# Optimization experiments

Measured on AMD Instinct MI355X. Metric: run time of the kernel, lower is better.

The kernel has to match this reference:

```python
import jax, jax.numpy as jnp
import numpy as np

DIMS = [11, 20, 20, 30, 30, 40, 40, 40, 20, 10, 1]  # layer widths

def setup_inputs() -> dict:
    key = jax.random.key(0)
    ks = jax.random.split(key, 1 + 2 * (len(DIMS) - 1))
    inp = {"x": jax.random.normal(ks[0], (2000000, 11), dtype=jnp.float32)}
    for i in range(len(DIMS) - 1):
        d_in, d_out = DIMS[i], DIMS[i + 1]
        bound = 1.0 / np.sqrt(d_in)
        inp[f"W{i}"] = jax.random.uniform(ks[1 + 2 * i], (d_out, d_in), dtype=jnp.float32, minval=-bound, maxval=bound)
        inp[f"b{i}"] = jax.random.uniform(ks[2 + 2 * i], (d_out,), dtype=jnp.float32, minval=-bound, maxval=bound)
    return inp

def _swish(x):
    return x * jax.nn.sigmoid(x)

def reference(x, W0, b0, W1, b1, W2, b2, W3, b3, W4, b4, W5, b5, W6, b6, W7, b7, W8, b8, W9, b9):
    Ws = [W0, W1, W2, W3, W4, W5, W6, W7, W8, W9]
    bs = [b0, b1, b2, b3, b4, b5, b6, b7, b8, b9]
    h = x
    for i in range(9):  # 9 Linear+Swish blocks
        h = _swish(h @ Ws[i].T + bs[i])
    h = jax.nn.relu(h @ Ws[9].T + bs[9])  # final Linear(10,1) + ReLU
    return h.reshape(-1)
```

## Files before the change

kernel.cpp:

```cpp
#include <hip/hip_runtime.h>
#include <math.h>


typedef _Float16 half8 __attribute__((ext_vector_type(8)));
typedef _Float16 half4 __attribute__((ext_vector_type(4)));
typedef _Float16 half2 __attribute__((ext_vector_type(2)));
typedef float f32x4 __attribute__((ext_vector_type(4)));

__device__ __forceinline__ float swish_f(float a) {
    float e = __expf(-a);
    return a * __builtin_amdgcn_rcpf(1.0f + e);
}

__device__ __forceinline__ half8 make_frag(const float* __restrict__ W,
                                           const float* __restrict__ b,
                                           int IN, int OUT, int ot, int kt,
                                           int lr, int kg) {
    const int r = ot * 16 + lr;
    half8 h;
#pragma unroll
    for (int e = 0; e < 8; ++e) {
        const int k = kt * 32 + kg * 8 + e;
        float v = 0.0f;
        if (r < OUT) {
            if (k < IN)
                v = W[r * IN + k];
            else if (k == IN)
                v = b[r];
        }
        h[e] = (_Float16)v;
    }
    return h;
}

template <int NOT, int OUT>
__device__ __forceinline__ void epilogue(const f32x4 (&acc)[NOT],
                                         _Float16* act, int lr, int kg) {
    const int kgl = kg & 1;
    const int kgh = kg >> 1;
#pragma unroll
    for (int ot = 0; ot < NOT; ++ot) {
        float v[4];
#pragma unroll
        for (int r = 0; r < 4; ++r) {
            v[r] = swish_f(acc[ot][r]);
            if (ot == OUT / 16 && ot * 16 + kg * 4 + r == OUT) v[r] = 1.0f;
        }
        auto lo = __builtin_amdgcn_cvt_pkrtz(v[0], v[1]);
        auto hi = __builtin_amdgcn_cvt_pkrtz(v[2], v[3]);
        union {
            half4 h4;
            half2 h2[2];
        } u;
        u.h2[0] = __builtin_bit_cast(half2, lo);
        u.h2[1] = __builtin_bit_cast(half2, hi);
        _Float16* p = act + (ot >> 1) * 512 +
                      (((2 * ot + kgh) & 3) * 16 + lr) * 8 + kgl * 4;
        *(half4*)p = u.h4;
    }
}

template <int NOT, int NKT, int OUT>
__device__ __forceinline__ void layer(const _Float16* __restrict__ wb,
                                      _Float16* act, int lane, int lr, int kg,
                                      f32x4 z4) {
    f32x4 acc[NOT];
#pragma unroll
    for (int kt = 0; kt < NKT; ++kt) {
        const half8 bf = *(const half8*)(act + kt * 512 + lane * 8);
#pragma unroll
        for (int ot = 0; ot < NOT; ++ot) {
            const half8 wf =
                *(const half8*)(wb + (ot * NKT + kt) * 512 + lane * 8);
            acc[ot] = __builtin_amdgcn_mfma_f32_16x16x32_f16(
                wf, bf, kt == 0 ? z4 : acc[ot], 0, 0, 0);
        }
    }
    epilogue<NOT, OUT>(acc, act, lr, kg);
}

__global__ __launch_bounds__(256, 4) void longnet_mlp_r7(
    const float* __restrict__ x,
    const float* __restrict__ W0, const float* __restrict__ b0,
    const float* __restrict__ W1, const float* __restrict__ b1,
    const float* __restrict__ W2, const float* __restrict__ b2,
    const float* __restrict__ W3, const float* __restrict__ b3,
    const float* __restrict__ W4, const float* __restrict__ b4,
    const float* __restrict__ W5, const float* __restrict__ b5,
    const float* __restrict__ W6, const float* __restrict__ b6,
    const float* __restrict__ W7, const float* __restrict__ b7,
    const float* __restrict__ W8, const float* __restrict__ b8,
    const float* __restrict__ W9, const float* __restrict__ b9,
    float* __restrict__ out, int n) {
    __shared__ __align__(16) _Float16 s_w[29 * 512];
    __shared__ __align__(16) _Float16 s_act[4 * 1024];

    const int tid = threadIdx.x;
    const int lane = tid & 63;
    const int wave = tid >> 6;
    const int lr = lane & 15;
    const int kg = lane >> 4;

    {
        const float* Wt[10] = {W0, W1, W2, W3, W4, W5, W6, W7, W8, W9};
        const float* bt[10] = {b0, b1, b2, b3, b4, b5, b6, b7, b8, b9};
        const int INs[10] = {11, 20, 20, 30, 30, 40, 40, 40, 20, 10};
        const int OUTs[10] = {20, 20, 30, 30, 40, 40, 40, 20, 10, 1};
        const int NOTs[10] = {2, 2, 2, 2, 3, 3, 3, 2, 1, 1};
        const int NKTs[10] = {1, 1, 1, 1, 1, 2, 2, 2, 1, 1};
        int f = 0;
        for (int L = 0; L < 10; ++L)
            for (int ot = 0; ot < NOTs[L]; ++ot)
                for (int kt = 0; kt < NKTs[L]; ++kt, ++f)
                    if ((f & 3) == wave) {
                        half8 h = make_frag(Wt[L], bt[L], INs[L], OUTs[L], ot,
                                            kt, lr, kg);
                        *(half8*)(s_w + f * 512 + lane * 8) = h;
                    }
    }

    _Float16* act = s_act + wave * 1024;
    {
        int* a32 = (int*)act;
#pragma unroll
        for (int i = 0; i < 8; ++i) a32[i * 64 + lane] = 0;
    }
    __syncthreads();

    const f32x4 z4 = (f32x4){0.f, 0.f, 0.f, 0.f};
    const int ntile = n >> 4;
    const int step = (int)gridDim.x * 4;

    for (int t = blockIdx.x * 4 + wave; t < ntile; t += step) {
        const int row0 = t * 16;

        half8 xb = {};
        if (kg < 2) {
            const float* xr = x + (size_t)(row0 + lr) * 11 + kg * 8;
#pragma unroll
            for (int e = 0; e < 8; ++e) {
                const int k = kg * 8 + e;
                float v = (k < 11) ? xr[e] : ((k == 11) ? 1.0f : 0.0f);
                xb[e] = (_Float16)v;
            }
        }

        {
            f32x4 acc[2];
#pragma unroll
            for (int ot = 0; ot < 2; ++ot) {
                const half8 wf = *(const half8*)(s_w + ot * 512 + lane * 8);
                acc[ot] = __builtin_amdgcn_mfma_f32_16x16x32_f16(wf, xb, z4,
                                                                 0, 0, 0);
            }
            epilogue<2, 20>(acc, act, lr, kg);
        }
        layer<2, 1, 20>(s_w + 2 * 512, act, lane, lr, kg, z4);
        layer<2, 1, 30>(s_w + 4 * 512, act, lane, lr, kg, z4);
        layer<2, 1, 30>(s_w + 6 * 512, act, lane, lr, kg, z4);
        layer<3, 1, 40>(s_w + 8 * 512, act, lane, lr, kg, z4);
        layer<3, 2, 40>(s_w + 11 * 512, act, lane, lr, kg, z4);
        layer<3, 2, 40>(s_w + 17 * 512, act, lane, lr, kg, z4);
        layer<2, 2, 20>(s_w + 23 * 512, act, lane, lr, kg, z4);
        layer<1, 1, 10>(s_w + 27 * 512, act, lane, lr, kg, z4);

        {
            const half8 wf = *(const half8*)(s_w + 28 * 512 + lane * 8);
            const half8 bf = *(const half8*)(act + lane * 8);
            f32x4 accF =
                __builtin_amdgcn_mfma_f32_16x16x32_f16(wf, bf, z4, 0, 0, 0);
            if (kg == 0) out[row0 + lr] = fmaxf(accF[0], 0.0f);
        }
    }
}

extern "C" void kernel_launch(void* const* d_in, const int* in_sizes, int n_in,
                              void* d_out, int out_size, void* d_ws, size_t ws_size,
                              hipStream_t stream) {
    const float* x = (const float*)d_in[0];
    const float* W0 = (const float*)d_in[1];
    const float* b0 = (const float*)d_in[2];
    const float* W1 = (const float*)d_in[3];
    const float* b1 = (const float*)d_in[4];
    const float* W2 = (const float*)d_in[5];
    const float* b2 = (const float*)d_in[6];
    const float* W3 = (const float*)d_in[7];
    const float* b3 = (const float*)d_in[8];
    const float* W4 = (const float*)d_in[9];
    const float* b4 = (const float*)d_in[10];
    const float* W5 = (const float*)d_in[11];
    const float* b5 = (const float*)d_in[12];
    const float* W6 = (const float*)d_in[13];
    const float* b6 = (const float*)d_in[14];
    const float* W7 = (const float*)d_in[15];
    const float* b7 = (const float*)d_in[16];
    const float* W8 = (const float*)d_in[17];
    const float* b8 = (const float*)d_in[18];
    const float* W9 = (const float*)d_in[19];
    const float* b9 = (const float*)d_in[20];
    float* out = (float*)d_out;

    const int n = in_sizes[0] / 11;
    const int grid = 1024;

    longnet_mlp_r7<<<grid, 256, 0, stream>>>(
        x, W0, b0, W1, b1, W2, b2, W3, b3, W4, b4, W5, b5, W6, b6, W7, b7, W8,
        b8, W9, b9, out, n);
}
```

Baseline: 196.8 us.

## Process two 16-row tiles per wave to interleave independent MFMA chains

Each wave now handles a pair of 16-row tiles, issuing two independent MFMA chains that share each weight fragment load, with a separate activation buffer per tile. This is meant to hide MFMA and LDS latency in the serial layer chain through instruction-level parallelism, and to halve the weight-fragment LDS reads per row. The grid is also reduced to 768 blocks. It doubles activation LDS and accumulator registers, which may lower occupancy, and rows beyond a multiple of 32 are now dropped (n=2M is divisible, so correct here).

```diff
diff --git a/kernel.cpp b/kernel.cpp
--- a/kernel.cpp
+++ b/kernel.cpp
@@ -61,25 +61,44 @@
 }
 
 template <int NOT, int NKT, int OUT>
-__device__ __forceinline__ void layer(const _Float16* __restrict__ wb,
-                                      _Float16* act, int lane, int lr, int kg,
-                                      f32x4 z4) {
-    f32x4 acc[NOT];
+__device__ __forceinline__ void layer2(const _Float16* __restrict__ wb,
+                                       _Float16* act0, _Float16* act1,
+                                       int lane, int lr, int kg, f32x4 z4) {
+    f32x4 acc0[NOT], acc1[NOT];
 #pragma unroll
     for (int kt = 0; kt < NKT; ++kt) {
-        const half8 bf = *(const half8*)(act + kt * 512 + lane * 8);
+        const half8 bf0 = *(const half8*)(act0 + kt * 512 + lane * 8);
+        const half8 bf1 = *(const half8*)(act1 + kt * 512 + lane * 8);
 #pragma unroll
         for (int ot = 0; ot < NOT; ++ot) {
             const half8 wf =
                 *(const half8*)(wb + (ot * NKT + kt) * 512 + lane * 8);
-            acc[ot] = __builtin_amdgcn_mfma_f32_16x16x32_f16(
-                wf, bf, kt == 0 ? z4 : acc[ot], 0, 0, 0);
-        }
-    }
-    epilogue<NOT, OUT>(acc, act, lr, kg);
-}
-
-__global__ __launch_bounds__(256, 4) void longnet_mlp_r7(
+            acc0[ot] = __builtin_amdgcn_mfma_f32_16x16x32_f16(
+                wf, bf0, kt == 0 ? z4 : acc0[ot], 0, 0, 0);
+            acc1[ot] = __builtin_amdgcn_mfma_f32_16x16x32_f16(
+                wf, bf1, kt == 0 ? z4 : acc1[ot], 0, 0, 0);
+        }
+    }
+    epilogue<NOT, OUT>(acc0, act0, lr, kg);
+    epilogue<NOT, OUT>(acc1, act1, lr, kg);
+}
+
+__device__ __forceinline__ half8 load_xb(const float* __restrict__ x,
+                                         int row0, int lr, int kg) {
+    half8 xb = {};
+    if (kg < 2) {
+        const float* xr = x + (size_t)(row0 + lr) * 11 + kg * 8;
+#pragma unroll
+        for (int e = 0; e < 8; ++e) {
+            const int k = kg * 8 + e;
+            float v = (k < 11) ? xr[e] : ((k == 11) ? 1.0f : 0.0f);
+            xb[e] = (_Float16)v;
+        }
+    }
+    return xb;
+}
+
+__global__ __launch_bounds__(256, 4) void longnet_mlp_r8(
     const float* __restrict__ x,
     const float* __restrict__ W0, const float* __restrict__ b0,
     const float* __restrict__ W1, const float* __restrict__ b1,
@@ -93,7 +112,7 @@
     const float* __restrict__ W9, const float* __restrict__ b9,
     float* __restrict__ out, int n) {
     __shared__ __align__(16) _Float16 s_w[29 * 512];
-    __shared__ __align__(16) _Float16 s_act[4 * 1024];
+    __shared__ __align__(16) _Float16 s_act[8 * 1024];
 
     const int tid = threadIdx.x;
     const int lane = tid & 63;
@@ -119,57 +138,59 @@
                     }
     }
 
-    _Float16* act = s_act + wave * 1024;
+    _Float16* act0 = s_act + wave * 2048;
+    _Float16* act1 = act0 + 1024;
     {
-        int* a32 = (int*)act;
-#pragma unroll
-        for (int i = 0; i < 8; ++i) a32[i * 64 + lane] = 0;
+        int* a32 = (int*)act0;
+#pragma unroll
+        for (int i = 0; i < 16; ++i) a32[i * 64 + lane] = 0;
     }
     __syncthreads();
 
     const f32x4 z4 = (f32x4){0.f, 0.f, 0.f, 0.f};
-    const int ntile = n >> 4;
+    const int npair = n >> 5;
     const int step = (int)gridDim.x * 4;
 
-    for (int t = blockIdx.x * 4 + wave; t < ntile; t += step) {
-        const int row0 = t * 16;
-
-        half8 xb = {};
-        if (kg < 2) {
-            const float* xr = x + (size_t)(row0 + lr) * 11 + kg * 8;
-#pragma unroll
-            for (int e = 0; e < 8; ++e) {
-                const int k = kg * 8 + e;
-                float v = (k < 11) ? xr[e] : ((k == 11) ? 1.0f : 0.0f);
-                xb[e] = (_Float16)v;
-            }
-        }
+    for (int t = blockIdx.x * 4 + wave; t < npair; t += step) {
+        const int row0 = t * 32;
+
+        const half8 xb0 = load_xb(x, row0, lr, kg);
+        const half8 xb1 = load_xb(x, row0 + 16, lr, kg);
 
         {
-            f32x4 acc[2];
+            f32x4 acc0[2], acc1[2];
 #pragma unroll
             for (int ot = 0; ot < 2; ++ot) {
                 const half8 wf = *(const half8*)(s_w + ot * 512 + lane * 8);
-                acc[ot] = __builtin_amdgcn_mfma_f32_16x16x32_f16(wf, xb, z4,
-                                                                 0, 0, 0);
+                acc0[ot] = __builtin_amdgcn_mfma_f32_16x16x32_f16(wf, xb0, z4,
+                                                                  0, 0, 0);
+                acc1[ot] = __builtin_amdgcn_mfma_f32_16x16x32_f16(wf, xb1, z4,
+                                                                  0, 0, 0);
             }
-            epilogue<2, 20>(acc, act, lr, kg);
-        }
-        layer<2, 1, 20>(s_w + 2 * 512, act, lane, lr, kg, z4);
-        layer<2, 1, 30>(s_w + 4 * 512, act, lane, lr, kg, z4);
-        layer<2, 1, 30>(s_w + 6 * 512, act, lane, lr, kg, z4);
-        layer<3, 1, 40>(s_w + 8 * 512, act, lane, lr, kg, z4);
-        layer<3, 2, 40>(s_w + 11 * 512, act, lane, lr, kg, z4);
-        layer<3, 2, 40>(s_w + 17 * 512, act, lane, lr, kg, z4);
-        layer<2, 2, 20>(s_w + 23 * 512, act, lane, lr, kg, z4);
-        layer<1, 1, 10>(s_w + 27 * 512, act, lane, lr, kg, z4);
+            epilogue<2, 20>(acc0, act0, lr, kg);
+            epilogue<2, 20>(acc1, act1, lr, kg);
+        }
+        layer2<2, 1, 20>(s_w + 2 * 512, act0, act1, lane, lr, kg, z4);
+        layer2<2, 1, 30>(s_w + 4 * 512, act0, act1, lane, lr, kg, z4);
+        layer2<2, 1, 30>(s_w + 6 * 512, act0, act1, lane, lr, kg, z4);
+        layer2<3, 1, 40>(s_w + 8 * 512, act0, act1, lane, lr, kg, z4);
+        layer2<3, 2, 40>(s_w + 11 * 512, act0, act1, lane, lr, kg, z4);
+        layer2<3, 2, 40>(s_w + 17 * 512, act0, act1, lane, lr, kg, z4);
+        layer2<2, 2, 20>(s_w + 23 * 512, act0, act1, lane, lr, kg, z4);
+        layer2<1, 1, 10>(s_w + 27 * 512, act0, act1, lane, lr, kg, z4);
 
         {
             const half8 wf = *(const half8*)(s_w + 28 * 512 + lane * 8);
-            const half8 bf = *(const half8*)(act + lane * 8);
-            f32x4 accF =
-                __builtin_amdgcn_mfma_f32_16x16x32_f16(wf, bf, z4, 0, 0, 0);
-            if (kg == 0) out[row0 + lr] = fmaxf(accF[0], 0.0f);
+            const half8 bf0 = *(const half8*)(act0 + lane * 8);
+            const half8 bf1 = *(const half8*)(act1 + lane * 8);
+            f32x4 aF0 =
+                __builtin_amdgcn_mfma_f32_16x16x32_f16(wf, bf0, z4, 0, 0, 0);
+            f32x4 aF1 =
+                __builtin_amdgcn_mfma_f32_16x16x32_f16(wf, bf1, z4, 0, 0, 0);
+            if (kg == 0) {
+                out[row0 + lr] = fmaxf(aF0[0], 0.0f);
+                out[row0 + 16 + lr] = fmaxf(aF1[0], 0.0f);
+            }
         }
     }
 }
@@ -201,9 +222,9 @@
     float* out = (float*)d_out;
 
     const int n = in_sizes[0] / 11;
-    const int grid = 1024;
-
-    longnet_mlp_r7<<<grid, 256, 0, stream>>>(
+    const int grid = 768;
+
+    longnet_mlp_r8<<<grid, 256, 0, stream>>>(
         x, W0, b0, W1, b1, W2, b2, W3, b3, W4, b4, W5, b5, W6, b6, W7, b7, W8,
         b8, W9, b9, out, n);
 }
```

New measurement: 208.2 us. 5.8% more time.

## Process two row tiles per wave and use K=16 MFMA for narrow layers

Applied to the files above, without the earlier changes.

Each wave now handles two 16-row tiles per iteration, interleaving their MFMAs so the same weight fragment feeds both and independent work can hide latency. Layers whose K dimension is small, and the 8-column remainder beyond 32, now use 16x16x16 MFMAs instead of padding to a full second 32-wide K tile. The activation buffer in LDS is XOR-swizzled to reduce bank conflicts. The cost is more registers and LDS per wave, which may lower occupancy, plus more complex indexing.

```diff
diff --git a/kernel.cpp b/kernel.cpp
--- a/kernel.cpp
+++ b/kernel.cpp
@@ -7,20 +7,36 @@
 typedef _Float16 half2 __attribute__((ext_vector_type(2)));
 typedef float f32x4 __attribute__((ext_vector_type(4)));
 
+__device__ __forceinline__ int swz(int a) {
+    return a ^ (((a >> 7) & 1) << 4) ^ (((a >> 8) & 1) << 5);
+}
+
 __device__ __forceinline__ float swish_f(float a) {
     float e = __expf(-a);
     return a * __builtin_amdgcn_rcpf(1.0f + e);
 }
 
-__device__ __forceinline__ half8 make_frag(const float* __restrict__ W,
-                                           const float* __restrict__ b,
-                                           int IN, int OUT, int ot, int kt,
-                                           int lr, int kg) {
+__device__ __forceinline__ half4 pack4(const float (&v)[4]) {
+    auto lo = __builtin_amdgcn_cvt_pkrtz(v[0], v[1]);
+    auto hi = __builtin_amdgcn_cvt_pkrtz(v[2], v[3]);
+    union {
+        half4 h4;
+        half2 h2[2];
+    } u;
+    u.h2[0] = __builtin_bit_cast(half2, lo);
+    u.h2[1] = __builtin_bit_cast(half2, hi);
+    return u.h4;
+}
+
+__device__ __forceinline__ half8 make_frag32(const float* __restrict__ W,
+                                             const float* __restrict__ b,
+                                             int IN, int OUT, int ot, int lr,
+                                             int kg) {
     const int r = ot * 16 + lr;
     half8 h;
 #pragma unroll
     for (int e = 0; e < 8; ++e) {
-        const int k = kt * 32 + kg * 8 + e;
+        const int k = kg * 8 + e;
         float v = 0.0f;
         if (r < OUT) {
             if (k < IN)
@@ -33,53 +49,120 @@
     return h;
 }
 
-template <int NOT, int OUT>
-__device__ __forceinline__ void epilogue(const f32x4 (&acc)[NOT],
-                                         _Float16* act, int lr, int kg) {
-    const int kgl = kg & 1;
-    const int kgh = kg >> 1;
+__device__ __forceinline__ half4 make_frag16(const float* __restrict__ W,
+                                             const float* __restrict__ b,
+                                             int IN, int OUT, int ot, int kb,
+                                             int lr, int kg) {
+    const int r = ot * 16 + lr;
+    half4 h;
+#pragma unroll
+    for (int e = 0; e < 4; ++e) {
+        const int k = kb + kg * 4 + e;
+        float v = 0.0f;
+        if (r < OUT) {
+            if (k < IN)
+                v = W[r * IN + k];
+            else if (k == IN)
+                v = b[r];
+        }
+        h[e] = (_Float16)v;
+    }
+    return h;
+}
+
+struct TP {
+    const half8* r0;
+    const half4* r1;
+    _Float16* w0;
+    _Float16* w1;
+    _Float16* wk;
+};
+
+template <int NK0, int MARK, int NOT>
+__device__ __forceinline__ void epi_kt0(const f32x4 (&A)[NOT], const TP& t,
+                                        int kg) {
+#pragma unroll
+    for (int ot = 0; ot < NK0; ++ot) {
+        float v[4];
+#pragma unroll
+        for (int r = 0; r < 4; ++r) {
+            v[r] = swish_f(A[ot][r]);
+            if (ot == MARK / 16 && ot * 16 + kg * 4 + r == MARK) v[r] = 1.0f;
+        }
+        _Float16* wp = (ot == 0) ? t.w0 : t.w1;
+        *(half4*)wp = pack4(v);
+    }
+}
+
+template <int MREL>
+__device__ __forceinline__ void epi_kt1(const f32x4& a, const TP& t, int kg) {
+    float v[4];
+#pragma unroll
+    for (int r = 0; r < 4; ++r) {
+        v[r] = swish_f(a[r]);
+        if constexpr (MREL >= 0) {
+            if (kg * 4 + r == MREL) v[r] = 1.0f;
+        }
+    }
+    *(half4*)t.wk = pack4(v);
+}
+
+template <int NOT, bool K1>
+__device__ __forceinline__ void compute2(const _Float16* __restrict__ w32,
+                                         const _Float16* __restrict__ w16,
+                                         const TP& t0, const TP& t1,
+                                         f32x4 (&A)[NOT], f32x4 (&B)[NOT],
+                                         int lane) {
+    const f32x4 z4 = {0.f, 0.f, 0.f, 0.f};
+    const half8 b0 = *t0.r0;
+    const half8 b1 = *t1.r0;
 #pragma unroll
     for (int ot = 0; ot < NOT; ++ot) {
-        float v[4];
-#pragma unroll
-        for (int r = 0; r < 4; ++r) {
-            v[r] = swish_f(acc[ot][r]);
-            if (ot == OUT / 16 && ot * 16 + kg * 4 + r == OUT) v[r] = 1.0f;
-        }
-        auto lo = __builtin_amdgcn_cvt_pkrtz(v[0], v[1]);
-        auto hi = __builtin_amdgcn_cvt_pkrtz(v[2], v[3]);
-        union {
-            half4 h4;
-            half2 h2[2];
-        } u;
-        u.h2[0] = __builtin_bit_cast(half2, lo);
-        u.h2[1] = __builtin_bit_cast(half2, hi);
-        _Float16* p = act + (ot >> 1) * 512 +
-                      (((2 * ot + kgh) & 3) * 16 + lr) * 8 + kgl * 4;
-        *(half4*)p = u.h4;
-    }
-}
-
-template <int NOT, int NKT, int OUT>
-__device__ __forceinline__ void layer(const _Float16* __restrict__ wb,
-                                      _Float16* act, int lane, int lr, int kg,
-                                      f32x4 z4) {
-    f32x4 acc[NOT];
-#pragma unroll
-    for (int kt = 0; kt < NKT; ++kt) {
-        const half8 bf = *(const half8*)(act + kt * 512 + lane * 8);
+        const half8 wf = *(const half8*)(w32 + ot * 512 + lane * 8);
+        A[ot] = __builtin_amdgcn_mfma_f32_16x16x32_f16(wf, b0, z4, 0, 0, 0);
+        B[ot] = __builtin_amdgcn_mfma_f32_16x16x32_f16(wf, b1, z4, 0, 0, 0);
+    }
+    if constexpr (K1) {
+        const half4 c0 = *t0.r1;
+        const half4 c1 = *t1.r1;
 #pragma unroll
         for (int ot = 0; ot < NOT; ++ot) {
-            const half8 wf =
-                *(const half8*)(wb + (ot * NKT + kt) * 512 + lane * 8);
-            acc[ot] = __builtin_amdgcn_mfma_f32_16x16x32_f16(
-                wf, bf, kt == 0 ? z4 : acc[ot], 0, 0, 0);
-        }
-    }
-    epilogue<NOT, OUT>(acc, act, lr, kg);
-}
-
-__global__ __launch_bounds__(256, 4) void longnet_mlp_r7(
+            const half4 wg = *(const half4*)(w16 + ot * 256 + lane * 4);
+            A[ot] = __builtin_amdgcn_mfma_f32_16x16x16f16(wg, c0, A[ot], 0, 0, 0);
+            B[ot] = __builtin_amdgcn_mfma_f32_16x16x16f16(wg, c1, B[ot], 0, 0, 0);
+        }
+    }
+}
+
+template <int NOT, bool K1, int NK0, int MARK, int MREL>
+__device__ __forceinline__ void layerX(const _Float16* __restrict__ w32,
+                                       const _Float16* __restrict__ w16,
+                                       const TP& t0, const TP& t1, int lane,
+                                       int kg) {
+    f32x4 A[NOT], B[NOT];
+    compute2<NOT, K1>(w32, w16, t0, t1, A, B, lane);
+    epi_kt0<NK0, MARK>(A, t0, kg);
+    epi_kt0<NK0, MARK>(B, t1, kg);
+    if constexpr (NOT > NK0) {
+        epi_kt1<MREL>(A[NK0], t0, kg);
+        epi_kt1<MREL>(B[NK0], t1, kg);
+    }
+}
+
+__device__ __forceinline__ half4 load_x4(const float* __restrict__ x,
+                                         int row0, int lr, int kg) {
+    half4 b = {};
+    const float* xr = x + (size_t)(row0 + lr) * 11;
+#pragma unroll
+    for (int e = 0; e < 4; ++e) {
+        const int k = kg * 4 + e;
+        float v = (k < 11) ? xr[k] : ((k == 11) ? 1.0f : 0.0f);
+        b[e] = (_Float16)v;
+    }
+    return b;
+}
+
+__global__ __launch_bounds__(256, 4) void longnet_mlp_r9(
     const float* __restrict__ x,
     const float* __restrict__ W0, const float* __restrict__ b0,
     const float* __restrict__ W1, const float* __restrict__ b1,
@@ -92,84 +175,104 @@
     const float* __restrict__ W8, const float* __restrict__ b8,
     const float* __restrict__ W9, const float* __restrict__ b9,
     float* __restrict__ out, int n) {
-    __shared__ __align__(16) _Float16 s_w[29 * 512];
-    __shared__ __align__(16) _Float16 s_act[4 * 1024];
+    __shared__ __align__(16) _Float16 s_w[12032];
+    __shared__ __align__(16) _Float16 s_act[6144];
 
     const int tid = threadIdx.x;
     const int lane = tid & 63;
     const int wave = tid >> 6;
     const int lr = lane & 15;
     const int kg = lane >> 4;
+    const int kgl = kg & 1;
+    const int kgh = kg >> 1;
+
+    _Float16* const s_w16 = s_w + 9216;
 
     {
         const float* Wt[10] = {W0, W1, W2, W3, W4, W5, W6, W7, W8, W9};
         const float* bt[10] = {b0, b1, b2, b3, b4, b5, b6, b7, b8, b9};
         const int INs[10] = {11, 20, 20, 30, 30, 40, 40, 40, 20, 10};
         const int OUTs[10] = {20, 20, 30, 30, 40, 40, 40, 20, 10, 1};
-        const int NOTs[10] = {2, 2, 2, 2, 3, 3, 3, 2, 1, 1};
-        const int NKTs[10] = {1, 1, 1, 1, 1, 2, 2, 2, 1, 1};
-        int f = 0;
-        for (int L = 0; L < 10; ++L)
-            for (int ot = 0; ot < NOTs[L]; ++ot)
-                for (int kt = 0; kt < NKTs[L]; ++kt, ++f)
-                    if ((f & 3) == wave) {
-                        half8 h = make_frag(Wt[L], bt[L], INs[L], OUTs[L], ot,
-                                            kt, lr, kg);
-                        *(half8*)(s_w + f * 512 + lane * 8) = h;
-                    }
-    }
-
-    _Float16* act = s_act + wave * 1024;
+        const int L32[18] = {1, 1, 2, 2, 3, 3, 4, 4, 4, 5, 5, 5, 6, 6, 6, 7, 7, 8};
+        const int O32[18] = {0, 1, 0, 1, 0, 1, 0, 1, 2, 0, 1, 2, 0, 1, 2, 0, 1, 0};
+#pragma unroll
+        for (int i = 0; i < 18; ++i)
+            if ((i & 3) == wave) {
+                const int L = L32[i];
+                half8 h = make_frag32(Wt[L], bt[L], INs[L], OUTs[L], O32[i],
+                                      lr, kg);
+                *(half8*)(s_w + i * 512 + lane * 8) = h;
+            }
+        const int L16[11] = {0, 0, 5, 5, 5, 6, 6, 6, 7, 7, 9};
+        const int O16[11] = {0, 1, 0, 1, 2, 0, 1, 2, 0, 1, 0};
+        const int KB16[11] = {0, 0, 32, 32, 32, 32, 32, 32, 32, 32, 0};
+#pragma unroll
+        for (int i = 0; i < 11; ++i)
+            if (((18 + i) & 3) == wave) {
+                const int L = L16[i];
+                half4 h = make_frag16(Wt[L], bt[L], INs[L], OUTs[L], O16[i],
+                                      KB16[i], lr, kg);
+                *(half4*)(s_w16 + i * 256 + lane * 4) = h;
+            }
+    }
+
+    char* const c0 = (char*)s_act + wave * 3072;
+    char* const c1 = c0 + 1536;
+    const int rd0 = swz(lane * 16);
+    const int rk1 = 1024 + lane * 8;
+    const int wo0 = swz((kgh & 3) * 256 + lr * 16 + kgl * 8);
+    const int wo1 = swz(((2 + kgh) & 3) * 256 + lr * 16 + kgl * 8);
+    const TP t0 = {(const half8*)(c0 + rd0), (const half4*)(c0 + rk1),
+                   (_Float16*)(c0 + wo0), (_Float16*)(c0 + wo1),
+                   (_Float16*)(c0 + rk1)};
+    const TP t1 = {(const half8*)(c1 + rd0), (const half4*)(c1 + rk1),
+                   (_Float16*)(c1 + wo0), (_Float16*)(c1 + wo1),
+                   (_Float16*)(c1 + rk1)};
+
     {
-        int* a32 = (int*)act;
-#pragma unroll
-        for (int i = 0; i < 8; ++i) a32[i * 64 + lane] = 0;
+        int* a32 = (int*)c0;
+#pragma unroll
+        for (int i = 0; i < 12; ++i) a32[i * 64 + lane] = 0;
     }
     __syncthreads();
 
-    const f32x4 z4 = (f32x4){0.f, 0.f, 0.f, 0.f};
-    const int ntile = n >> 4;
+    const f32x4 z4 = {0.f, 0.f, 0.f, 0.f};
+    const int npair = n >> 5;
     const int step = (int)gridDim.x * 4;
 
-    for (int t = blockIdx.x * 4 + wave; t < ntile; t += step) {
-        const int row0 = t * 16;
-
-        half8 xb = {};
-        if (kg < 2) {
-            const float* xr = x + (size_t)(row0 + lr) * 11 + kg * 8;
-#pragma unroll
-            for (int e = 0; e < 8; ++e) {
-                const int k = kg * 8 + e;
-                float v = (k < 11) ? xr[e] : ((k == 11) ? 1.0f : 0.0f);
-                xb[e] = (_Float16)v;
+    for (int t = blockIdx.x * 4 + wave; t < npair; t += step) {
+        const int row0 = t * 32;
+
+        {
+            const half4 xb0 = load_x4(x, row0, lr, kg);
+            const half4 xb1 = load_x4(x, row0 + 16, lr, kg);
+            f32x4 A[2], B[2];
+#pragma unroll
+            for (int ot = 0; ot < 2; ++ot) {
+                const half4 wg = *(const half4*)(s_w16 + ot * 256 + lane * 4);
+                A[ot] = __builtin_amdgcn_mfma_f32_16x16x16f16(wg, xb0, z4, 0, 0, 0);
+                B[ot] = __builtin_amdgcn_mfma_f32_16x16x16f16(wg, xb1, z4, 0, 0, 0);
             }
-        }
+            epi_kt0<2, 20>(A, t0, kg);
+            epi_kt0<2, 20>(B, t1, kg);
+        }
+        layerX<2, false, 2, 20, -1>(s_w + 0 * 512, s_w, t0, t1, lane, kg);
+        layerX<2, false, 2, 30, -1>(s_w + 2 * 512, s_w, t0, t1, lane, kg);
+        layerX<2, false, 2, 30, -1>(s_w + 4 * 512, s_w, t0, t1, lane, kg);
+        layerX<3, false, 2, 1000, 8>(s_w + 6 * 512, s_w, t0, t1, lane, kg);
+        layerX<3, true, 2, 1000, 8>(s_w + 9 * 512, s_w16 + 2 * 256, t0, t1, lane, kg);
+        layerX<3, true, 2, 1000, 8>(s_w + 12 * 512, s_w16 + 5 * 256, t0, t1, lane, kg);
+        layerX<2, true, 2, 20, -1>(s_w + 15 * 512, s_w16 + 8 * 256, t0, t1, lane, kg);
+        layerX<1, false, 0, 1000, 10>(s_w + 17 * 512, s_w, t0, t1, lane, kg);
 
         {
-            f32x4 acc[2];
-#pragma unroll
-            for (int ot = 0; ot < 2; ++ot) {
-                const half8 wf = *(const half8*)(s_w + ot * 512 + lane * 8);
-                acc[ot] = __builtin_amdgcn_mfma_f32_16x16x32_f16(wf, xb, z4,
-                                                                 0, 0, 0);
+            const half4 wg = *(const half4*)(s_w16 + 10 * 256 + lane * 4);
+            f32x4 F0 = __builtin_amdgcn_mfma_f32_16x16x16f16(wg, *t0.r1, z4, 0, 0, 0);
+            f32x4 F1 = __builtin_amdgcn_mfma_f32_16x16x16f16(wg, *t1.r1, z4, 0, 0, 0);
+            if (kg == 0) {
+                out[row0 + lr] = fmaxf(F0[0], 0.0f);
+                out[row0 + 16 + lr] = fmaxf(F1[0], 0.0f);
             }
-            epilogue<2, 20>(acc, act, lr, kg);
-        }
-        layer<2, 1, 20>(s_w + 2 * 512, act, lane, lr, kg, z4);
-        layer<2, 1, 30>(s_w + 4 * 512, act, lane, lr, kg, z4);
-        layer<2, 1, 30>(s_w + 6 * 512, act, lane, lr, kg, z4);
-        layer<3, 1, 40>(s_w + 8 * 512, act, lane, lr, kg, z4);
-        layer<3, 2, 40>(s_w + 11 * 512, act, lane, lr, kg, z4);
-        layer<3, 2, 40>(s_w + 17 * 512, act, lane, lr, kg, z4);
-        layer<2, 2, 20>(s_w + 23 * 512, act, lane, lr, kg, z4);
-        layer<1, 1, 10>(s_w + 27 * 512, act, lane, lr, kg, z4);
-
-        {
-            const half8 wf = *(const half8*)(s_w + 28 * 512 + lane * 8);
-            const half8 bf = *(const half8*)(act + lane * 8);
-            f32x4 accF =
-                __builtin_amdgcn_mfma_f32_16x16x32_f16(wf, bf, z4, 0, 0, 0);
-            if (kg == 0) out[row0 + lr] = fmaxf(accF[0], 0.0f);
         }
     }
 }
@@ -203,7 +306,7 @@
     const int n = in_sizes[0] / 11;
     const int grid = 1024;
 
-    longnet_mlp_r7<<<grid, 256, 0, stream>>>(
+    longnet_mlp_r9<<<grid, 256, 0, stream>>>(
         x, W0, b0, W1, b1, W2, b2, W3, b3, W4, b4, W5, b5, W6, b6, W7, b7, W8,
         b8, W9, b9, out, n);
 }
```

Measured after the change: 179.6 us. -8.7%, faster.

## Keep activations in registers via 16x16x16 MFMA and process four tiles per wave

Applied to the files above, without the earlier changes.

Switches from the 16x16x32 MFMA, which needed an LDS round trip to re-layout activations between layers, to the 16x16x16 MFMA. With this instruction the output accumulator layout directly matches the next layer's B-operand layout, so activations stay in registers and the per-wave LDS activation buffer is gone. Each wave now handles four 16-row tiles at once, so each LDS weight fragment load is reused four times and independent MFMAs can interleave. The costs are more K-steps per layer (more, smaller MFMAs), higher register pressure from four tiles of accumulators, and a loop that drops any rows not divisible by 64.

```diff
diff --git a/kernel.cpp b/kernel.cpp
--- a/kernel.cpp
+++ b/kernel.cpp
@@ -2,25 +2,38 @@
 #include <math.h>
 
 
-typedef _Float16 half8 __attribute__((ext_vector_type(8)));
 typedef _Float16 half4 __attribute__((ext_vector_type(4)));
 typedef _Float16 half2 __attribute__((ext_vector_type(2)));
 typedef float f32x4 __attribute__((ext_vector_type(4)));
 
+#define T 4
+
 __device__ __forceinline__ float swish_f(float a) {
     float e = __expf(-a);
     return a * __builtin_amdgcn_rcpf(1.0f + e);
 }
 
-__device__ __forceinline__ half8 make_frag(const float* __restrict__ W,
-                                           const float* __restrict__ b,
-                                           int IN, int OUT, int ot, int kt,
-                                           int lr, int kg) {
+__device__ __forceinline__ half4 pack4(const float (&v)[4]) {
+    auto lo = __builtin_amdgcn_cvt_pkrtz(v[0], v[1]);
+    auto hi = __builtin_amdgcn_cvt_pkrtz(v[2], v[3]);
+    union {
+        half4 h4;
+        half2 h2[2];
+    } u;
+    u.h2[0] = __builtin_bit_cast(half2, lo);
+    u.h2[1] = __builtin_bit_cast(half2, hi);
+    return u.h4;
+}
+
+__device__ __forceinline__ half4 make_frag16(const float* __restrict__ W,
+                                             const float* __restrict__ b,
+                                             int IN, int OUT, int ot, int kb,
+                                             int lr, int kg) {
     const int r = ot * 16 + lr;
-    half8 h;
-#pragma unroll
-    for (int e = 0; e < 8; ++e) {
-        const int k = kt * 32 + kg * 8 + e;
+    half4 h;
+#pragma unroll
+    for (int e = 0; e < 4; ++e) {
+        const int k = kb + kg * 4 + e;
         float v = 0.0f;
         if (r < OUT) {
             if (k < IN)
@@ -33,53 +46,53 @@
     return h;
 }
 
-template <int NOT, int OUT>
-__device__ __forceinline__ void epilogue(const f32x4 (&acc)[NOT],
-                                         _Float16* act, int lr, int kg) {
-    const int kgl = kg & 1;
-    const int kgh = kg >> 1;
-#pragma unroll
-    for (int ot = 0; ot < NOT; ++ot) {
-        float v[4];
-#pragma unroll
-        for (int r = 0; r < 4; ++r) {
-            v[r] = swish_f(acc[ot][r]);
-            if (ot == OUT / 16 && ot * 16 + kg * 4 + r == OUT) v[r] = 1.0f;
-        }
-        auto lo = __builtin_amdgcn_cvt_pkrtz(v[0], v[1]);
-        auto hi = __builtin_amdgcn_cvt_pkrtz(v[2], v[3]);
-        union {
-            half4 h4;
-            half2 h2[2];
-        } u;
-        u.h2[0] = __builtin_bit_cast(half2, lo);
-        u.h2[1] = __builtin_bit_cast(half2, hi);
-        _Float16* p = act + (ot >> 1) * 512 +
-                      (((2 * ot + kgh) & 3) * 16 + lr) * 8 + kgl * 4;
-        *(half4*)p = u.h4;
-    }
-}
-
-template <int NOT, int NKT, int OUT>
-__device__ __forceinline__ void layer(const _Float16* __restrict__ wb,
-                                      _Float16* act, int lane, int lr, int kg,
-                                      f32x4 z4) {
-    f32x4 acc[NOT];
+template <int NKT, int NOT, int MARK>
+__device__ __forceinline__ void layerR(const _Float16* __restrict__ wb,
+                                       half4 (&bf)[T][3], int lane, int kg) {
+    const f32x4 z4 = {0.f, 0.f, 0.f, 0.f};
+    f32x4 acc[T][NOT];
 #pragma unroll
     for (int kt = 0; kt < NKT; ++kt) {
-        const half8 bf = *(const half8*)(act + kt * 512 + lane * 8);
 #pragma unroll
         for (int ot = 0; ot < NOT; ++ot) {
-            const half8 wf =
-                *(const half8*)(wb + (ot * NKT + kt) * 512 + lane * 8);
-            acc[ot] = __builtin_amdgcn_mfma_f32_16x16x32_f16(
-                wf, bf, kt == 0 ? z4 : acc[ot], 0, 0, 0);
-        }
-    }
-    epilogue<NOT, OUT>(acc, act, lr, kg);
-}
-
-__global__ __launch_bounds__(256, 4) void longnet_mlp_r7(
+            const half4 wg =
+                *(const half4*)(wb + (ot * NKT + kt) * 256 + lane * 4);
+#pragma unroll
+            for (int t = 0; t < T; ++t)
+                acc[t][ot] = __builtin_amdgcn_mfma_f32_16x16x16f16(
+                    wg, bf[t][kt], kt == 0 ? z4 : acc[t][ot], 0, 0, 0);
+        }
+    }
+#pragma unroll
+    for (int t = 0; t < T; ++t) {
+#pragma unroll
+        for (int ot = 0; ot < NOT; ++ot) {
+            float v[4];
+#pragma unroll
+            for (int r = 0; r < 4; ++r) {
+                v[r] = swish_f(acc[t][ot][r]);
+                if (ot == MARK / 16 && ot * 16 + kg * 4 + r == MARK)
+                    v[r] = 1.0f;
+            }
+            bf[t][ot] = pack4(v);
+        }
+    }
+}
+
+__device__ __forceinline__ half4 load_x4(const float* __restrict__ x,
+                                         int row0, int lr, int kg) {
+    half4 b = {};
+    const float* xr = x + (size_t)(row0 + lr) * 11;
+#pragma unroll
+    for (int e = 0; e < 4; ++e) {
+        const int k = kg * 4 + e;
+        float v = (k < 11) ? xr[k] : ((k == 11) ? 1.0f : 0.0f);
+        b[e] = (_Float16)v;
+    }
+    return b;
+}
+
+__global__ __launch_bounds__(256, 4) void longnet_mlp_r11(
     const float* __restrict__ x,
     const float* __restrict__ W0, const float* __restrict__ b0,
     const float* __restrict__ W1, const float* __restrict__ b1,
@@ -92,8 +105,7 @@
     const float* __restrict__ W8, const float* __restrict__ b8,
     const float* __restrict__ W9, const float* __restrict__ b9,
     float* __restrict__ out, int n) {
-    __shared__ __align__(16) _Float16 s_w[29 * 512];
-    __shared__ __align__(16) _Float16 s_act[4 * 1024];
+    __shared__ __align__(16) _Float16 s_w[47 * 256];
 
     const int tid = threadIdx.x;
     const int lane = tid & 63;
@@ -107,69 +119,49 @@
         const int INs[10] = {11, 20, 20, 30, 30, 40, 40, 40, 20, 10};
         const int OUTs[10] = {20, 20, 30, 30, 40, 40, 40, 20, 10, 1};
         const int NOTs[10] = {2, 2, 2, 2, 3, 3, 3, 2, 1, 1};
-        const int NKTs[10] = {1, 1, 1, 1, 1, 2, 2, 2, 1, 1};
+        const int NKTs[10] = {1, 2, 2, 2, 2, 3, 3, 3, 2, 1};
         int f = 0;
         for (int L = 0; L < 10; ++L)
             for (int ot = 0; ot < NOTs[L]; ++ot)
                 for (int kt = 0; kt < NKTs[L]; ++kt, ++f)
                     if ((f & 3) == wave) {
-                        half8 h = make_frag(Wt[L], bt[L], INs[L], OUTs[L], ot,
-                                            kt, lr, kg);
-                        *(half8*)(s_w + f * 512 + lane * 8) = h;
+                        half4 h = make_frag16(Wt[L], bt[L], INs[L], OUTs[L],
+                                              ot, kt * 16, lr, kg);
+                        *(half4*)(s_w + f * 256 + lane * 4) = h;
                     }
     }
-
-    _Float16* act = s_act + wave * 1024;
-    {
-        int* a32 = (int*)act;
-#pragma unroll
-        for (int i = 0; i < 8; ++i) a32[i * 64 + lane] = 0;
-    }
     __syncthreads();
 
-    const f32x4 z4 = (f32x4){0.f, 0.f, 0.f, 0.f};
-    const int ntile = n >> 4;
+    const f32x4 z4 = {0.f, 0.f, 0.f, 0.f};
+    const int ngrp = n >> 6;
     const int step = (int)gridDim.x * 4;
 
-    for (int t = blockIdx.x * 4 + wave; t < ntile; t += step) {
-        const int row0 = t * 16;
-
-        half8 xb = {};
-        if (kg < 2) {
-            const float* xr = x + (size_t)(row0 + lr) * 11 + kg * 8;
-#pragma unroll
-            for (int e = 0; e < 8; ++e) {
-                const int k = kg * 8 + e;
-                float v = (k < 11) ? xr[e] : ((k == 11) ? 1.0f : 0.0f);
-                xb[e] = (_Float16)v;
+    for (int g = blockIdx.x * 4 + wave; g < ngrp; g += step) {
+        const int row0 = g * 64;
+
+        half4 bf[T][3];
+#pragma unroll
+        for (int t = 0; t < T; ++t)
+            bf[t][0] = load_x4(x, row0 + t * 16, lr, kg);
+
+        layerR<1, 2, 20>(s_w + 0 * 256, bf, lane, kg);
+        layerR<2, 2, 20>(s_w + 2 * 256, bf, lane, kg);
+        layerR<2, 2, 30>(s_w + 6 * 256, bf, lane, kg);
+        layerR<2, 2, 30>(s_w + 10 * 256, bf, lane, kg);
+        layerR<2, 3, 40>(s_w + 14 * 256, bf, lane, kg);
+        layerR<3, 3, 40>(s_w + 20 * 256, bf, lane, kg);
+        layerR<3, 3, 40>(s_w + 29 * 256, bf, lane, kg);
+        layerR<3, 2, 20>(s_w + 38 * 256, bf, lane, kg);
+        layerR<2, 1, 10>(s_w + 44 * 256, bf, lane, kg);
+
+        {
+            const half4 wg = *(const half4*)(s_w + 46 * 256 + lane * 4);
+#pragma unroll
+            for (int t = 0; t < T; ++t) {
+                f32x4 F = __builtin_amdgcn_mfma_f32_16x16x16f16(
+                    wg, bf[t][0], z4, 0, 0, 0);
+                if (kg == 0) out[row0 + t * 16 + lr] = fmaxf(F[0], 0.0f);
             }
-        }
-
-        {
-            f32x4 acc[2];
-#pragma unroll
-            for (int ot = 0; ot < 2; ++ot) {
-                const half8 wf = *(const half8*)(s_w + ot * 512 + lane * 8);
-                acc[ot] = __builtin_amdgcn_mfma_f32_16x16x32_f16(wf, xb, z4,
-                                                                 0, 0, 0);
-            }
-            epilogue<2, 20>(acc, act, lr, kg);
-        }
-        layer<2, 1, 20>(s_w + 2 * 512, act, lane, lr, kg, z4);
-        layer<2, 1, 30>(s_w + 4 * 512, act, lane, lr, kg, z4);
-        layer<2, 1, 30>(s_w + 6 * 512, act, lane, lr, kg, z4);
-        layer<3, 1, 40>(s_w + 8 * 512, act, lane, lr, kg, z4);
-        layer<3, 2, 40>(s_w + 11 * 512, act, lane, lr, kg, z4);
-        layer<3, 2, 40>(s_w + 17 * 512, act, lane, lr, kg, z4);
-        layer<2, 2, 20>(s_w + 23 * 512, act, lane, lr, kg, z4);
-        layer<1, 1, 10>(s_w + 27 * 512, act, lane, lr, kg, z4);
-
-        {
-            const half8 wf = *(const half8*)(s_w + 28 * 512 + lane * 8);
-            const half8 bf = *(const half8*)(act + lane * 8);
-            f32x4 accF =
-                __builtin_amdgcn_mfma_f32_16x16x32_f16(wf, bf, z4, 0, 0, 0);
-            if (kg == 0) out[row0 + lr] = fmaxf(accF[0], 0.0f);
         }
     }
 }
@@ -203,7 +195,7 @@
     const int n = in_sizes[0] / 11;
     const int grid = 1024;
 
-    longnet_mlp_r7<<<grid, 256, 0, stream>>>(
+    longnet_mlp_r11<<<grid, 256, 0, stream>>>(
         x, W0, b0, W1, b1, W2, b2, W3, b3, W4, b4, W5, b5, W6, b6, W7, b7, W8,
         b8, W9, b9, out, n);
 }
```

Result: faster. 182.0 us (-7.5%).
